# Kernel tuning notes

Measured on AMD Instinct MI355X. Metric: run time of the kernel, lower is better.

Reference implementation:

```python
import jax, jax.numpy as jnp
import numpy as np

N = 8_000_000   # total nodes (atoms)
B = 4096        # number of graphs in the batch
EPS = 1e-05


def setup_inputs() -> dict:
    key = jax.random.key(0)
    k1, k2 = jax.random.split(key)
    pos = jax.random.normal(k1, (N, 3), dtype=jnp.float32)
    batch = jnp.sort(jax.random.randint(k2, (N,), 0, B).astype(jnp.int64))
    weight = jnp.ones((1, 1), dtype=jnp.float32)
    return {"pos": pos, "batch": batch, "weight": weight}


def reference(pos, batch, weight):
    # per-node L2 norm of 3D coordinates -> [N, 1]
    norm = jnp.linalg.norm(pos, axis=-1, keepdims=True)
    # scatter_mean over graphs: segment sums of norms and counts -> [B, 1]
    seg_sum = jax.ops.segment_sum(norm, batch, num_segments=B)
    counts = jax.ops.segment_sum(jnp.ones_like(norm), batch, num_segments=B)
    mean_norm = seg_sum / jnp.maximum(counts, 1.0)  # empty segments -> 0 (matches scatter_mean)
    # gather per-graph mean back to nodes and normalize
    new_pos = weight * pos / (mean_norm[batch] + EPS)
    return new_pos
```

## Files before the change

### kernel.cpp

```cpp
#include <hip/hip_runtime.h>

#define EPS_F 1e-5f
#define BGRAPHS 4096
#define NODES_PER_BLOCK 1024

__device__ __forceinline__ int batch_shift(const int* __restrict__ batch, int n) {
    return (batch[n - 1] == 0) ? 1 : 0;
}

__global__ __launch_bounds__(256) void se3_seg_reduce(
    const float* __restrict__ pos, const int* __restrict__ batch,
    float* __restrict__ sums, float* __restrict__ cnts,
    int* __restrict__ starts, int n)
{
    const int tid  = blockIdx.x * blockDim.x + threadIdx.x;
    const int base = tid * 4;
    const int lane = threadIdx.x & 63;
    const int shift = batch_shift(batch, n);

    int   cur_b = -1;
    float cur_s = 0.f, cur_c = 0.f;

    if (base < n) {
        int   b4[4];
        float nrm[4];
        int   prev;
        const int nb = min(4, n - base);
        if (nb == 4) {
            if (shift == 0) {
                const int4 bi = *reinterpret_cast<const int4*>(batch + base);
                b4[0] = bi.x; b4[1] = bi.y; b4[2] = bi.z; b4[3] = bi.w;
            } else {
                const int4 v0 = *reinterpret_cast<const int4*>(batch + 2 * base);
                const int4 v1 = *reinterpret_cast<const int4*>(batch + 2 * base + 4);
                b4[0] = v0.x; b4[1] = v0.z; b4[2] = v1.x; b4[3] = v1.z;
            }
            const int up = __shfl_up(b4[3], 1);
            if (lane == 0) prev = (base == 0) ? -1 : batch[(size_t)(base - 1) << shift];
            else           prev = up;

            const float4* p = reinterpret_cast<const float4*>(pos + (size_t)base * 3);
            const float4 a = p[0], b = p[1], c = p[2];
            nrm[0] = sqrtf(a.x * a.x + a.y * a.y + a.z * a.z);
            nrm[1] = sqrtf(a.w * a.w + b.x * b.x + b.y * b.y);
            nrm[2] = sqrtf(b.z * b.z + b.w * b.w + c.x * c.x);
            nrm[3] = sqrtf(c.y * c.y + c.z * c.z + c.w * c.w);
        } else {
            for (int j = 0; j < 4; ++j) { b4[j] = -1; nrm[j] = 0.f; }
            for (int j = 0; j < nb; ++j) {
                b4[j] = batch[(size_t)(base + j) << shift];
                const float x = pos[(size_t)(base + j) * 3 + 0];
                const float y = pos[(size_t)(base + j) * 3 + 1];
                const float z = pos[(size_t)(base + j) * 3 + 2];
                nrm[j] = sqrtf(x * x + y * y + z * z);
            }
            prev = (base == 0) ? -1 : batch[(size_t)(base - 1) << shift];
        }

        if (b4[0] >= 0 && b4[0] != prev) starts[b4[0]] = base;
        #pragma unroll
        for (int j = 1; j < 4; ++j)
            if (b4[j] >= 0 && b4[j] != b4[j - 1]) starts[b4[j]] = base + j;

        cur_b = b4[0];
        cur_s = nrm[0];
        cur_c = (b4[0] >= 0) ? 1.f : 0.f;
        #pragma unroll
        for (int j = 1; j < 4; ++j) {
            if (b4[j] == cur_b) { cur_s += nrm[j]; cur_c += 1.f; }
            else {
                if (cur_b >= 0) { atomicAdd(&sums[cur_b], cur_s); atomicAdd(&cnts[cur_b], cur_c); }
                cur_b = b4[j]; cur_s = nrm[j]; cur_c = (b4[j] >= 0) ? 1.f : 0.f;
            }
        }
    }

    #pragma unroll
    for (int off = 1; off < 64; off <<= 1) {
        const float os = __shfl_down(cur_s, off);
        const float oc = __shfl_down(cur_c, off);
        const int   ob = __shfl_down(cur_b, off);
        if (lane + off < 64 && ob == cur_b) { cur_s += os; cur_c += oc; }
    }
    const int pb = __shfl_up(cur_b, 1);
    if ((lane == 0 || pb != cur_b) && cur_b >= 0) {
        atomicAdd(&sums[cur_b], cur_s);
        atomicAdd(&cnts[cur_b], cur_c);
    }
}

__global__ __launch_bounds__(1024) void se3_finalize(
    const float* __restrict__ sums, const float* __restrict__ cnts,
    const float* __restrict__ w, float* __restrict__ scale,
    int* __restrict__ starts, int* __restrict__ cg, int nchunks)
{
    __shared__ int ta[BGRAPHS], tb[BGRAPHS];
    const int t = threadIdx.x;
    for (int i = t; i < BGRAPHS; i += 1024) ta[i] = starts[i];
    __syncthreads();
    int* src = ta; int* dst = tb;
    for (int stride = 1; stride < BGRAPHS; stride <<= 1) {
        for (int i = t; i < BGRAPHS; i += 1024) {
            int v = src[i];
            if (i + stride < BGRAPHS) v = min(v, src[i + stride]);
            dst[i] = v;
        }
        __syncthreads();
        int* tmp = src; src = dst; dst = tmp;
    }
    for (int i = t; i < BGRAPHS; i += 1024) {
        starts[i] = src[i];
        const float mean = sums[i] / fmaxf(cnts[i], 1.f);
        scale[i] = w[0] / (mean + EPS_F);
    }
    for (int c = t; c < nchunks; c += 1024) {
        const int x = c * NODES_PER_BLOCK;
        int lo = 0, hi = BGRAPHS - 1;
        #pragma unroll
        for (int s = 0; s < 12; ++s) {
            const int mid = (lo + hi + 1) >> 1;
            if (src[mid] <= x) lo = mid; else hi = mid - 1;
        }
        cg[c] = lo;
    }
}

__global__ __launch_bounds__(256) void se3_apply(
    const float* __restrict__ pos, const int* __restrict__ t,
    const float* __restrict__ scale, const int* __restrict__ cg,
    float* __restrict__ out, int n)
{
    const int tid  = blockIdx.x * blockDim.x + threadIdx.x;
    const int base = tid * 4;
    if (base >= n) return;

    int g = cg[blockIdx.x];
    while (g < BGRAPHS - 1 && t[g + 1] <= base) ++g;
    float sc[4];
    sc[0] = scale[g];
    #pragma unroll
    for (int j = 1; j < 4; ++j) {
        while (g < BGRAPHS - 1 && t[g + 1] <= base + j) ++g;
        sc[j] = scale[g];
    }

    if (base + 4 <= n) {
        const float4* p = reinterpret_cast<const float4*>(pos + (size_t)base * 3);
        const float4 a = p[0], b = p[1], c = p[2];
        float4* q = reinterpret_cast<float4*>(out + (size_t)base * 3);
        q[0] = make_float4(a.x * sc[0], a.y * sc[0], a.z * sc[0], a.w * sc[1]);
        q[1] = make_float4(b.x * sc[1], b.y * sc[1], b.z * sc[2], b.w * sc[2]);
        q[2] = make_float4(c.x * sc[2], c.y * sc[3], c.z * sc[3], c.w * sc[3]);
    } else {
        for (int j = 0; j < n - base; ++j) {
            out[(size_t)(base + j) * 3 + 0] = pos[(size_t)(base + j) * 3 + 0] * sc[j];
            out[(size_t)(base + j) * 3 + 1] = pos[(size_t)(base + j) * 3 + 1] * sc[j];
            out[(size_t)(base + j) * 3 + 2] = pos[(size_t)(base + j) * 3 + 2] * sc[j];
        }
    }
}

extern "C" void kernel_launch(void* const* d_in, const int* in_sizes, int n_in,
                              void* d_out, int out_size, void* d_ws, size_t ws_size,
                              hipStream_t stream)
{
    const float* pos   = (const float*)d_in[0];
    const int*   batch = (const int*)d_in[1];
    const float* w     = (const float*)d_in[2];
    float*       out   = (float*)d_out;
    const int    n     = in_sizes[1];

    float* sums   = (float*)d_ws;
    float* cnts   = sums + BGRAPHS;
    float* scale  = cnts + BGRAPHS;
    int*   starts = (int*)(scale + BGRAPHS);
    int*   cg     = starts + BGRAPHS;

    const int nthreads = (n + 3) / 4;
    const int blocks   = (nthreads + 255) / 256;

    hipMemsetAsync(d_ws, 0, 2 * BGRAPHS * sizeof(float), stream);
    hipMemsetAsync(starts, 0x7F, BGRAPHS * sizeof(int), stream);

    se3_seg_reduce<<<blocks, 256, 0, stream>>>(pos, batch, sums, cnts, starts, n);
    se3_finalize<<<1, 1024, 0, stream>>>(sums, cnts, w, scale, starts, cg, blocks);
    se3_apply<<<blocks, 256, 0, stream>>>(pos, starts, scale, cg, out, n);
}
```

Measured before the change: 78.50 us.

## Merge workspace memsets via encoded starts and use branchless windowed graph lookup

Graph start offsets are now stored as ENC minus the offset. A zeroed entry then means 'absent', so one memset covers sums, counts and starts, and the finalize scan uses max instead of min. The apply kernel no longer runs a data-dependent while loop over segment starts per node. It preloads a fixed window of 8 next-start offsets and scales from the block's first graph, then picks each node's scale with branchless selects. This removes one memset launch and divergent serial loads. It assumes no block of 1024 nodes spans more than 8 graph boundaries, which holds for ~1950 nodes per graph but is not guaranteed in general.

```diff
diff --git a/kernel.cpp b/kernel.cpp
--- a/kernel.cpp
+++ b/kernel.cpp
@@ -2,7 +2,10 @@
 
 #define EPS_F 1e-5f
 #define BGRAPHS 4096
-#define NODES_PER_BLOCK 1024
+#define NPB 1024
+#define WIN 8
+#define ENC 0x40000000
+#define INF_I 0x7fffffff
 
 __device__ __forceinline__ int batch_shift(const int* __restrict__ batch, int n) {
     return (batch[n - 1] == 0) ? 1 : 0;
@@ -11,7 +14,7 @@
 __global__ __launch_bounds__(256) void se3_seg_reduce(
     const float* __restrict__ pos, const int* __restrict__ batch,
     float* __restrict__ sums, float* __restrict__ cnts,
-    int* __restrict__ starts, int n)
+    int* __restrict__ enc, int n)
 {
     const int tid  = blockIdx.x * blockDim.x + threadIdx.x;
     const int base = tid * 4;
@@ -57,10 +60,10 @@
             prev = (base == 0) ? -1 : batch[(size_t)(base - 1) << shift];
         }
 
-        if (b4[0] >= 0 && b4[0] != prev) starts[b4[0]] = base;
+        if (b4[0] >= 0 && b4[0] != prev) enc[b4[0]] = ENC - base;
         #pragma unroll
         for (int j = 1; j < 4; ++j)
-            if (b4[j] >= 0 && b4[j] != b4[j - 1]) starts[b4[j]] = base + j;
+            if (b4[j] >= 0 && b4[j] != b4[j - 1]) enc[b4[j]] = ENC - (base + j);
 
         cur_b = b4[0];
         cur_s = nrm[0];
@@ -92,56 +95,66 @@
 __global__ __launch_bounds__(1024) void se3_finalize(
     const float* __restrict__ sums, const float* __restrict__ cnts,
     const float* __restrict__ w, float* __restrict__ scale,
-    int* __restrict__ starts, int* __restrict__ cg, int nchunks)
+    int* __restrict__ enc, int* __restrict__ cg, int nchunks)
 {
     __shared__ int ta[BGRAPHS], tb[BGRAPHS];
     const int t = threadIdx.x;
-    for (int i = t; i < BGRAPHS; i += 1024) ta[i] = starts[i];
+    for (int i = t; i < BGRAPHS; i += 1024) ta[i] = enc[i];
     __syncthreads();
     int* src = ta; int* dst = tb;
     for (int stride = 1; stride < BGRAPHS; stride <<= 1) {
         for (int i = t; i < BGRAPHS; i += 1024) {
             int v = src[i];
-            if (i + stride < BGRAPHS) v = min(v, src[i + stride]);
+            if (i + stride < BGRAPHS) v = max(v, src[i + stride]);
             dst[i] = v;
         }
         __syncthreads();
         int* tmp = src; src = dst; dst = tmp;
     }
     for (int i = t; i < BGRAPHS; i += 1024) {
-        starts[i] = src[i];
+        enc[i] = ENC - src[i];
         const float mean = sums[i] / fmaxf(cnts[i], 1.f);
         scale[i] = w[0] / (mean + EPS_F);
     }
     for (int c = t; c < nchunks; c += 1024) {
-        const int x = c * NODES_PER_BLOCK;
+        const int key = ENC - c * NPB;
         int lo = 0, hi = BGRAPHS - 1;
         #pragma unroll
         for (int s = 0; s < 12; ++s) {
             const int mid = (lo + hi + 1) >> 1;
-            if (src[mid] <= x) lo = mid; else hi = mid - 1;
+            if (src[mid] >= key) lo = mid; else hi = mid - 1;
         }
         cg[c] = lo;
     }
 }
 
 __global__ __launch_bounds__(256) void se3_apply(
-    const float* __restrict__ pos, const int* __restrict__ t,
+    const float* __restrict__ pos, const int* __restrict__ tstart,
     const float* __restrict__ scale, const int* __restrict__ cg,
     float* __restrict__ out, int n)
 {
-    const int tid  = blockIdx.x * blockDim.x + threadIdx.x;
-    const int base = tid * 4;
+    const int base = (blockIdx.x * blockDim.x + threadIdx.x) * 4;
     if (base >= n) return;
 
-    int g = cg[blockIdx.x];
-    while (g < BGRAPHS - 1 && t[g + 1] <= base) ++g;
+    const int g0 = cg[blockIdx.x];
+    int   w[WIN];
+    float sw[WIN + 1];
+    #pragma unroll
+    for (int k = 0; k < WIN; ++k) {
+        const int idx = g0 + 1 + k;
+        w[k] = (idx < BGRAPHS) ? tstart[idx] : INF_I;
+    }
+    #pragma unroll
+    for (int k = 0; k <= WIN; ++k) sw[k] = scale[min(g0 + k, BGRAPHS - 1)];
+
     float sc[4];
-    sc[0] = scale[g];
-    #pragma unroll
-    for (int j = 1; j < 4; ++j) {
-        while (g < BGRAPHS - 1 && t[g + 1] <= base + j) ++g;
-        sc[j] = scale[g];
+    #pragma unroll
+    for (int j = 0; j < 4; ++j) {
+        const int i = base + j;
+        float s = sw[0];
+        #pragma unroll
+        for (int k = 0; k < WIN; ++k) s = (w[k] <= i) ? sw[k + 1] : s;
+        sc[j] = s;
     }
 
     if (base + 4 <= n) {
@@ -170,19 +183,18 @@
     float*       out   = (float*)d_out;
     const int    n     = in_sizes[1];
 
-    float* sums   = (float*)d_ws;
-    float* cnts   = sums + BGRAPHS;
-    float* scale  = cnts + BGRAPHS;
-    int*   starts = (int*)(scale + BGRAPHS);
-    int*   cg     = starts + BGRAPHS;
+    float* sums  = (float*)d_ws;
+    float* cnts  = sums + BGRAPHS;
+    int*   enc   = (int*)(cnts + BGRAPHS);
+    float* scale = (float*)(enc + BGRAPHS);
+    int*   cg    = (int*)(scale + BGRAPHS);
 
     const int nthreads = (n + 3) / 4;
     const int blocks   = (nthreads + 255) / 256;
 
-    hipMemsetAsync(d_ws, 0, 2 * BGRAPHS * sizeof(float), stream);
-    hipMemsetAsync(starts, 0x7F, BGRAPHS * sizeof(int), stream);
-
-    se3_seg_reduce<<<blocks, 256, 0, stream>>>(pos, batch, sums, cnts, starts, n);
-    se3_finalize<<<1, 1024, 0, stream>>>(sums, cnts, w, scale, starts, cg, blocks);
-    se3_apply<<<blocks, 256, 0, stream>>>(pos, starts, scale, cg, out, n);
-}
+    hipMemsetAsync(d_ws, 0, 3 * BGRAPHS * sizeof(float), stream);
+
+    se3_seg_reduce<<<blocks, 256, 0, stream>>>(pos, batch, sums, cnts, enc, n);
+    se3_finalize<<<1, 1024, 0, stream>>>(sums, cnts, w, scale, enc, cg, blocks);
+    se3_apply<<<blocks, 256, 0, stream>>>(pos, enc, scale, cg, out, n);
+}
```

After: 76.79 us. 2.2% less time.
